# Performance work log

Hardware: AMD Instinct MI355X
Metric: run time of the kernel (lower is better)

Reference implementation:

```python
import jax, jax.numpy as jnp
import numpy as np


def setup_inputs() -> dict:
    key = jax.random.key(0)
    k1, k2 = jax.random.split(key)
    z = jax.random.normal(k1, (16, 128, 32, 32), dtype=jnp.float32)
    e = jax.random.normal(k2, (8192, 128), dtype=jnp.float32)
    log_sigma = jnp.zeros((1,), dtype=jnp.float32)  # init_log_sigma = 0.0
    return {"z": z, "e": e, "log_sigma": log_sigma}


def reference(z, e, log_sigma):
    # z: [B, C, H, W] latents; e: [M, C] codebook; log_sigma: [1]
    B, C, H, W = z.shape
    zf = jnp.transpose(z, (0, 2, 3, 1)).reshape(-1, C)  # [N, C]
    N = zf.shape[0]
    M = e.shape[0]
    T = 1.0  # latent_temp default

    # squared L2 distance via expanded dot products: ||z||^2 + ||e||^2 - 2 z.e
    z_sq = jnp.sum(zf * zf, axis=1, keepdims=True)          # [N, 1]
    e_sq = jnp.sum(e * e, axis=1)[None, :]                  # [1, M]
    dist = jnp.maximum(z_sq + e_sq - 2.0 * (zf @ e.T), 0.0)  # [N, M]

    alpha = -1.0 / (2.0 * jnp.exp(log_sigma[0]) ** 2)
    A = alpha * dist / T                                     # [N, M]

    # np.log(np.e) == 1.0 in the original
    const = 0.5 * C * (2.0 * log_sigma - 1.0)                # [1]
    lse1_loss = -jnp.mean(T * jax.nn.logsumexp(A, axis=1)) + const + jnp.log(float(M))
    lse2_loss = -jnp.mean(T * jax.nn.logsumexp(A, axis=0)) + const + jnp.log(float(N))
    return lse1_loss, lse2_loss
```

## Files before the change

kernel.cpp:

```cpp
#include <hip/hip_runtime.h>
#include <hip/hip_bf16.h>

typedef unsigned short u16;
typedef __attribute__((ext_vector_type(8))) short short8;
typedef __attribute__((ext_vector_type(4))) float float4v;
typedef __attribute__((ext_vector_type(2))) float float2v;

#define N_ROWS 16384
#define M_COLS 8192
#define KDIM   128
#define SHIFT  64.0f
#define STRIPES 64
#define SPLITS  64
#define CHUNKS  4

__device__ inline u16 f2bf(float f) {
  unsigned u = __builtin_bit_cast(unsigned, f);
  unsigned r = (u + 0x7fffu + ((u >> 16) & 1u)) >> 16;
  return (u16)r;
}

__global__ void prep(const float* __restrict__ z, const float* __restrict__ e,
                     u16* __restrict__ zf, u16* __restrict__ ef,
                     float* __restrict__ zsq, float* __restrict__ esq,
                     double* __restrict__ dacc, unsigned* __restrict__ dcnt) {
  if (blockIdx.x < 512) {
    const int b = blockIdx.x >> 5, h = blockIdx.x & 31;
    __shared__ float tile[128 * 33];
    __shared__ float psum[8][32];
    const float* src = z + ((size_t)b * 128 * 32 + h) * 32;
    for (int idx = threadIdx.x; idx < 4096; idx += 256) {
      int c = idx >> 5, w = idx & 31;
      tile[c * 33 + w] = src[c * 1024 + w];
    }
    __syncthreads();
    {
      int w = threadIdx.x & 31, cg = threadIdx.x >> 5;
      float s = 0.f;
#pragma unroll
      for (int cc = 0; cc < 16; ++cc) {
        float v = tile[(cg * 16 + cc) * 33 + w];
        s = fmaf(v, v, s);
      }
      psum[cg][w] = s;
    }
    for (int idx = threadIdx.x; idx < 512; idx += 256) {
      int w = idx >> 4, g = idx & 15;
      short8 v;
#pragma unroll
      for (int cc = 0; cc < 8; ++cc) v[cc] = (short)f2bf(tile[(g * 8 + cc) * 33 + w]);
      *(short8*)&zf[((size_t)b * 1024 + h * 32 + w) * 128 + g * 8] = v;
    }
    __syncthreads();
    if (threadIdx.x < 32) {
      int w = threadIdx.x;
      float s = 0.f;
#pragma unroll
      for (int cg = 0; cg < 8; ++cg) s += psum[cg][w];
      zsq[b * 1024 + h * 32 + w] = s;
    }
  } else {
    if (blockIdx.x == 512 && threadIdx.x == 0) {
      __hip_atomic_store(&dacc[0], 0.0, __ATOMIC_RELAXED, __HIP_MEMORY_SCOPE_AGENT);
      __hip_atomic_store(&dacc[1], 0.0, __ATOMIC_RELAXED, __HIP_MEMORY_SCOPE_AGENT);
      __hip_atomic_store(dcnt, 0u, __ATOMIC_RELAXED, __HIP_MEMORY_SCOPE_AGENT);
    }
    const int gw = ((blockIdx.x - 512) * 256 + threadIdx.x) >> 6;
    const int ln = threadIdx.x & 63;
    for (int r = gw; r < M_COLS; r += 512) {
      float2 v = *(const float2*)&e[r * 128 + ln * 2];
      unsigned pk = (unsigned)f2bf(v.x) | ((unsigned)f2bf(v.y) << 16);
      *(unsigned*)&ef[r * 128 + ln * 2] = pk;
      float s = fmaf(v.x, v.x, v.y * v.y);
#pragma unroll
      for (int sh = 1; sh < 64; sh <<= 1) s += __shfl_xor(s, sh);
      if (ln == 0) esq[r] = s;
    }
  }
}

__global__ __launch_bounds__(256, 3) void gemm_lse(
    const u16* __restrict__ zf, const u16* __restrict__ ef,
    const float* __restrict__ zsq, const float* __restrict__ esq,
    const float* __restrict__ log_sigma,
    float* __restrict__ rpart, float* __restrict__ cpart) {
  __shared__ __align__(16) u16 et[128 * 128];
  __shared__ float colacc[4][128];
  const int tid = threadIdx.x;
  const int ln = tid & 63, wv = tid >> 6;
  const int l15 = ln & 15, q = ln >> 4;
  const int stripe = blockIdx.x, split = blockIdx.y;
  const int colbase = split * 128;

  {
    const u16* efb = ef + (size_t)colbase * 128;
#pragma unroll
    for (int it = 0; it < 8; ++it) {
      int u = it * 256 + tid;
      int r = u >> 4, p_ = u & 15;
      int g = p_ ^ (r & 15);
      __builtin_amdgcn_global_load_lds(
          (const __attribute__((address_space(1))) unsigned int*)(efb + r * 128 + g * 8),
          (__attribute__((address_space(3))) unsigned int*)(et + (it * 256 + wv * 64) * 8),
          16, 0, 0);
    }
  }

  short8 af[4][4];
#pragma unroll
  for (int i = 0; i < 4; ++i)
#pragma unroll
    for (int kk = 0; kk < 4; ++kk)
      af[i][kk] = *(const short8*)(zf +
          (size_t)(stripe * 256 + wv * 64 + i * 16 + l15) * 128 + kk * 32 + q * 8);

  const float lsv = log_sigma[0];
  const float sg = __expf(lsv);
  const float alpha = -0.5f / (sg * sg);
  const float L2E = 1.44269504088896f;
  const float ca = alpha * L2E, cb = SHIFT * L2E, m2ca = -2.0f * ca;
  const float2v m2ca2 = {m2ca, m2ca};

  float2v zb2[4][2];
#pragma unroll
  for (int i = 0; i < 4; ++i) {
    float4v zs = *(const float4v*)(zsq + stripe * 256 + wv * 64 + i * 16 + q * 4);
    zb2[i][0] = (float2v){fmaf(ca, zs[0], cb), fmaf(ca, zs[1], cb)};
    zb2[i][1] = (float2v){fmaf(ca, zs[2], cb), fmaf(ca, zs[3], cb)};
  }

  float2v rs01[4], rs23[4];
#pragma unroll
  for (int i = 0; i < 4; ++i) {
    rs01[i] = (float2v){0.f, 0.f};
    rs23[i] = (float2v){0.f, 0.f};
  }

  __syncthreads();

#pragma unroll 1
  for (int t = 0; t < CHUNKS; ++t) {
    float ebv[2];
#pragma unroll
    for (int j = 0; j < 2; ++j) ebv[j] = ca * esq[colbase + t * 32 + j * 16 + l15];

    const u16* bb = et + t * 32 * 128;

    float4v acc[4][2];
#pragma unroll
    for (int kk = 0; kk < 4; ++kk) {
      short8 bfr[2];
      const int poff = ((kk * 4 + q) ^ l15) * 8;
#pragma unroll
      for (int j = 0; j < 2; ++j)
        bfr[j] = *(const short8*)(bb + (j * 16 + l15) * 128 + poff);
      if (kk == 0) {
#pragma unroll
        for (int i = 0; i < 4; ++i)
#pragma unroll
          for (int j = 0; j < 2; ++j)
            acc[i][j] = __builtin_amdgcn_mfma_f32_16x16x32_bf16(
                af[i][0], bfr[j], (float4v){0.f, 0.f, 0.f, 0.f}, 0, 0, 0);
      } else {
#pragma unroll
        for (int i = 0; i < 4; ++i)
#pragma unroll
          for (int j = 0; j < 2; ++j)
            acc[i][j] = __builtin_amdgcn_mfma_f32_16x16x32_bf16(
                af[i][kk], bfr[j], acc[i][j], 0, 0, 0);
      }
    }

    float2v csv[2];
    csv[0] = (float2v){0.f, 0.f};
    csv[1] = (float2v){0.f, 0.f};

#pragma unroll
    for (int i = 0; i < 4; ++i) {
#pragma unroll
      for (int j = 0; j < 2; ++j) {
        float2v eb2 = {ebv[j], ebv[j]};
        float2v a01 = {acc[i][j][0], acc[i][j][1]};
        float2v a23 = {acc[i][j][2], acc[i][j][3]};
        float2v g01 = a01 * m2ca2 + (zb2[i][0] + eb2);
        float2v g23 = a23 * m2ca2 + (zb2[i][1] + eb2);
        float2v e01 = {__builtin_amdgcn_exp2f(g01.x), __builtin_amdgcn_exp2f(g01.y)};
        float2v e23 = {__builtin_amdgcn_exp2f(g23.x), __builtin_amdgcn_exp2f(g23.y)};
        rs01[i] += e01;
        rs23[i] += e23;
        csv[j] += e01 + e23;
      }
    }
#pragma unroll
    for (int j = 0; j < 2; ++j) {
      float c = csv[j].x + csv[j].y;
      c += __shfl_xor(c, 16);
      c += __shfl_xor(c, 32);
      if (q == 0) colacc[wv][t * 32 + j * 16 + l15] = c;
    }
  }

  __syncthreads();
  if (tid < 128) {
    float s = 0.f;
#pragma unroll
    for (int w = 0; w < 4; ++w) s += colacc[w][tid];
    cpart[(size_t)stripe * M_COLS + colbase + tid] = s;
  }

#pragma unroll
  for (int i = 0; i < 4; ++i)
    for (int s = 1; s < 16; s <<= 1) {
      rs01[i].x += __shfl_xor(rs01[i].x, s);
      rs01[i].y += __shfl_xor(rs01[i].y, s);
      rs23[i].x += __shfl_xor(rs23[i].x, s);
      rs23[i].y += __shfl_xor(rs23[i].y, s);
    }
  if (l15 == 0) {
#pragma unroll
    for (int i = 0; i < 4; ++i) {
      int rbase = stripe * 256 + wv * 64 + i * 16 + q * 4;
      rpart[(size_t)split * N_ROWS + rbase + 0] = rs01[i].x;
      rpart[(size_t)split * N_ROWS + rbase + 1] = rs01[i].y;
      rpart[(size_t)split * N_ROWS + rbase + 2] = rs23[i].x;
      rpart[(size_t)split * N_ROWS + rbase + 3] = rs23[i].y;
    }
  }
}

__global__ void fin(const float* __restrict__ rpart, const float* __restrict__ cpart,
                    const float* __restrict__ log_sigma,
                    double* __restrict__ dacc, unsigned* __restrict__ dcnt,
                    float* __restrict__ out) {
  const int tid = threadIdx.x, b = blockIdx.x;
  double v;
  if (b < 64) {
    int row = b * 256 + tid;
    float s = 0.f;
#pragma unroll
    for (int p = 0; p < SPLITS; ++p) s += rpart[(size_t)p * N_ROWS + row];
    v = (double)logf(s);
  } else {
    int col = (b - 64) * 256 + tid;
    float s = 0.f;
#pragma unroll
    for (int p = 0; p < STRIPES; ++p) s += cpart[(size_t)p * M_COLS + col];
    v = (double)logf(s);
  }
  __shared__ double red[256];
  red[tid] = v;
  __syncthreads();
  for (int s = 128; s > 0; s >>= 1) {
    if (tid < s) red[tid] += red[tid + s];
    __syncthreads();
  }
  if (tid == 0) {
    atomicAdd(&dacc[b < 64 ? 0 : 1], red[0]);
    __threadfence();
    unsigned ticket = atomicAdd(dcnt, 1u);
    if (ticket == 95u) {
      double s1 = atomicAdd(&dacc[0], 0.0);
      double s2 = atomicAdd(&dacc[1], 0.0);
      float lsv = log_sigma[0];
      float cst = 0.5f * 128.0f * (2.0f * lsv - 1.0f);
      out[0] = (float)(-(s1 / N_ROWS - (double)SHIFT)) + cst + logf((float)M_COLS);
      out[1] = (float)(-(s2 / M_COLS - (double)SHIFT)) + cst + logf((float)N_ROWS);
    }
  }
}

extern "C" void kernel_launch(void* const* d_in, const int* in_sizes, int n_in,
                              void* d_out, int out_size, void* d_ws, size_t ws_size,
                              hipStream_t stream) {
  const float* z  = (const float*)d_in[0];
  const float* e  = (const float*)d_in[1];
  const float* ls = (const float*)d_in[2];
  float* out = (float*)d_out;
  char* ws = (char*)d_ws;
  u16*   zf    = (u16*)ws;
  u16*   ef    = (u16*)(ws + (4u << 20));
  float* zsq   = (float*)(ws + (6u << 20));
  float* esq   = (float*)(ws + (6u << 20) + (64u << 10));
  float* rpart = (float*)(ws + (6u << 20) + (96u << 10));
  float* cpart = (float*)(ws + (10u << 20) + (96u << 10));
  double* dacc = (double*)(ws + (12u << 20) + (96u << 10));
  unsigned* dcnt = (unsigned*)(ws + (12u << 20) + (96u << 10) + 16);

  prep<<<dim3(640), dim3(256), 0, stream>>>(z, e, zf, ef, zsq, esq, dacc, dcnt);
  gemm_lse<<<dim3(STRIPES, SPLITS), dim3(256), 0, stream>>>(zf, ef, zsq, esq, ls, rpart, cpart);
  fin<<<dim3(96), dim3(256), 0, stream>>>(rpart, cpart, ls, dacc, dcnt, out);
}
```

Baseline: 153.9 us.

## Halve GEMM-LSE tile to 128x64, raise occupancy, store partial sums as bf16

Each gemm_lse block now covers 128 rows by 64 codebook columns instead of 256x128, giving a 128x128 grid. The smaller LDS tile and register footprint allow launch bounds of 5 blocks per CU. Row and column partial exp-sums are stored as bf16 to offset the doubled count of partials the finalize kernel must read. Risks: more blocks redo the codebook staging and A-fragment loads, and bf16 rounding of the partials reduces accuracy of the final logsumexp.

```diff
diff --git a/kernel.cpp b/kernel.cpp
--- a/kernel.cpp
+++ b/kernel.cpp
@@ -10,14 +10,18 @@
 #define M_COLS 8192
 #define KDIM   128
 #define SHIFT  64.0f
-#define STRIPES 64
-#define SPLITS  64
-#define CHUNKS  4
+#define STRIPES 128
+#define SPLITS  128
+#define CHUNKS  2
 
 __device__ inline u16 f2bf(float f) {
   unsigned u = __builtin_bit_cast(unsigned, f);
   unsigned r = (u + 0x7fffu + ((u >> 16) & 1u)) >> 16;
   return (u16)r;
+}
+__device__ inline float bf2f(u16 h) {
+  unsigned u = ((unsigned)h) << 16;
+  return __builtin_bit_cast(float, u);
 }
 
 __global__ void prep(const float* __restrict__ z, const float* __restrict__ e,
@@ -79,23 +83,23 @@
   }
 }
 
-__global__ __launch_bounds__(256, 3) void gemm_lse(
+__global__ __launch_bounds__(256, 5) void gemm_lse(
     const u16* __restrict__ zf, const u16* __restrict__ ef,
     const float* __restrict__ zsq, const float* __restrict__ esq,
     const float* __restrict__ log_sigma,
-    float* __restrict__ rpart, float* __restrict__ cpart) {
-  __shared__ __align__(16) u16 et[128 * 128];
-  __shared__ float colacc[4][128];
+    u16* __restrict__ rpart, u16* __restrict__ cpart) {
+  __shared__ __align__(16) u16 et[64 * 128];
+  __shared__ float colacc[4][64];
   const int tid = threadIdx.x;
   const int ln = tid & 63, wv = tid >> 6;
   const int l15 = ln & 15, q = ln >> 4;
   const int stripe = blockIdx.x, split = blockIdx.y;
-  const int colbase = split * 128;
+  const int colbase = split * 64;
 
   {
     const u16* efb = ef + (size_t)colbase * 128;
 #pragma unroll
-    for (int it = 0; it < 8; ++it) {
+    for (int it = 0; it < 4; ++it) {
       int u = it * 256 + tid;
       int r = u >> 4, p_ = u & 15;
       int g = p_ ^ (r & 15);
@@ -106,13 +110,13 @@
     }
   }
 
-  short8 af[4][4];
-#pragma unroll
-  for (int i = 0; i < 4; ++i)
+  short8 af[2][4];
+#pragma unroll
+  for (int i = 0; i < 2; ++i)
 #pragma unroll
     for (int kk = 0; kk < 4; ++kk)
       af[i][kk] = *(const short8*)(zf +
-          (size_t)(stripe * 256 + wv * 64 + i * 16 + l15) * 128 + kk * 32 + q * 8);
+          (size_t)(stripe * 128 + wv * 32 + i * 16 + l15) * 128 + kk * 32 + q * 8);
 
   const float lsv = log_sigma[0];
   const float sg = __expf(lsv);
@@ -121,17 +125,17 @@
   const float ca = alpha * L2E, cb = SHIFT * L2E, m2ca = -2.0f * ca;
   const float2v m2ca2 = {m2ca, m2ca};
 
-  float2v zb2[4][2];
-#pragma unroll
-  for (int i = 0; i < 4; ++i) {
-    float4v zs = *(const float4v*)(zsq + stripe * 256 + wv * 64 + i * 16 + q * 4);
+  float2v zb2[2][2];
+#pragma unroll
+  for (int i = 0; i < 2; ++i) {
+    float4v zs = *(const float4v*)(zsq + stripe * 128 + wv * 32 + i * 16 + q * 4);
     zb2[i][0] = (float2v){fmaf(ca, zs[0], cb), fmaf(ca, zs[1], cb)};
     zb2[i][1] = (float2v){fmaf(ca, zs[2], cb), fmaf(ca, zs[3], cb)};
   }
 
-  float2v rs01[4], rs23[4];
-#pragma unroll
-  for (int i = 0; i < 4; ++i) {
+  float2v rs01[2], rs23[2];
+#pragma unroll
+  for (int i = 0; i < 2; ++i) {
     rs01[i] = (float2v){0.f, 0.f};
     rs23[i] = (float2v){0.f, 0.f};
   }
@@ -146,7 +150,7 @@
 
     const u16* bb = et + t * 32 * 128;
 
-    float4v acc[4][2];
+    float4v acc[2][2];
 #pragma unroll
     for (int kk = 0; kk < 4; ++kk) {
       short8 bfr[2];
@@ -156,14 +160,14 @@
         bfr[j] = *(const short8*)(bb + (j * 16 + l15) * 128 + poff);
       if (kk == 0) {
 #pragma unroll
-        for (int i = 0; i < 4; ++i)
+        for (int i = 0; i < 2; ++i)
 #pragma unroll
           for (int j = 0; j < 2; ++j)
             acc[i][j] = __builtin_amdgcn_mfma_f32_16x16x32_bf16(
                 af[i][0], bfr[j], (float4v){0.f, 0.f, 0.f, 0.f}, 0, 0, 0);
       } else {
 #pragma unroll
-        for (int i = 0; i < 4; ++i)
+        for (int i = 0; i < 2; ++i)
 #pragma unroll
           for (int j = 0; j < 2; ++j)
             acc[i][j] = __builtin_amdgcn_mfma_f32_16x16x32_bf16(
@@ -176,14 +180,16 @@
     csv[1] = (float2v){0.f, 0.f};
 
 #pragma unroll
-    for (int i = 0; i < 4; ++i) {
+    for (int i = 0; i < 2; ++i) {
 #pragma unroll
       for (int j = 0; j < 2; ++j) {
         float2v eb2 = {ebv[j], ebv[j]};
+        float2v zbeb01 = zb2[i][0] + eb2;
+        float2v zbeb23 = zb2[i][1] + eb2;
         float2v a01 = {acc[i][j][0], acc[i][j][1]};
         float2v a23 = {acc[i][j][2], acc[i][j][3]};
-        float2v g01 = a01 * m2ca2 + (zb2[i][0] + eb2);
-        float2v g23 = a23 * m2ca2 + (zb2[i][1] + eb2);
+        float2v g01 = a01 * m2ca2 + zbeb01;
+        float2v g23 = a23 * m2ca2 + zbeb23;
         float2v e01 = {__builtin_amdgcn_exp2f(g01.x), __builtin_amdgcn_exp2f(g01.y)};
         float2v e23 = {__builtin_amdgcn_exp2f(g23.x), __builtin_amdgcn_exp2f(g23.y)};
         rs01[i] += e01;
@@ -201,15 +207,15 @@
   }
 
   __syncthreads();
-  if (tid < 128) {
+  if (tid < 64) {
     float s = 0.f;
 #pragma unroll
     for (int w = 0; w < 4; ++w) s += colacc[w][tid];
-    cpart[(size_t)stripe * M_COLS + colbase + tid] = s;
-  }
-
-#pragma unroll
-  for (int i = 0; i < 4; ++i)
+    cpart[(size_t)stripe * M_COLS + colbase + tid] = f2bf(s);
+  }
+
+#pragma unroll
+  for (int i = 0; i < 2; ++i)
     for (int s = 1; s < 16; s <<= 1) {
       rs01[i].x += __shfl_xor(rs01[i].x, s);
       rs01[i].y += __shfl_xor(rs01[i].y, s);
@@ -218,17 +224,17 @@
     }
   if (l15 == 0) {
 #pragma unroll
-    for (int i = 0; i < 4; ++i) {
-      int rbase = stripe * 256 + wv * 64 + i * 16 + q * 4;
-      rpart[(size_t)split * N_ROWS + rbase + 0] = rs01[i].x;
-      rpart[(size_t)split * N_ROWS + rbase + 1] = rs01[i].y;
-      rpart[(size_t)split * N_ROWS + rbase + 2] = rs23[i].x;
-      rpart[(size_t)split * N_ROWS + rbase + 3] = rs23[i].y;
-    }
-  }
-}
-
-__global__ void fin(const float* __restrict__ rpart, const float* __restrict__ cpart,
+    for (int i = 0; i < 2; ++i) {
+      int rbase = stripe * 128 + wv * 32 + i * 16 + q * 4;
+      rpart[(size_t)split * N_ROWS + rbase + 0] = f2bf(rs01[i].x);
+      rpart[(size_t)split * N_ROWS + rbase + 1] = f2bf(rs01[i].y);
+      rpart[(size_t)split * N_ROWS + rbase + 2] = f2bf(rs23[i].x);
+      rpart[(size_t)split * N_ROWS + rbase + 3] = f2bf(rs23[i].y);
+    }
+  }
+}
+
+__global__ void fin(const u16* __restrict__ rpart, const u16* __restrict__ cpart,
                     const float* __restrict__ log_sigma,
                     double* __restrict__ dacc, unsigned* __restrict__ dcnt,
                     float* __restrict__ out) {
@@ -238,13 +244,13 @@
     int row = b * 256 + tid;
     float s = 0.f;
 #pragma unroll
-    for (int p = 0; p < SPLITS; ++p) s += rpart[(size_t)p * N_ROWS + row];
+    for (int p = 0; p < SPLITS; ++p) s += bf2f(rpart[(size_t)p * N_ROWS + row]);
     v = (double)logf(s);
   } else {
     int col = (b - 64) * 256 + tid;
     float s = 0.f;
 #pragma unroll
-    for (int p = 0; p < STRIPES; ++p) s += cpart[(size_t)p * M_COLS + col];
+    for (int p = 0; p < STRIPES; ++p) s += bf2f(cpart[(size_t)p * M_COLS + col]);
     v = (double)logf(s);
   }
   __shared__ double red[256];
@@ -281,8 +287,8 @@
   u16*   ef    = (u16*)(ws + (4u << 20));
   float* zsq   = (float*)(ws + (6u << 20));
   float* esq   = (float*)(ws + (6u << 20) + (64u << 10));
-  float* rpart = (float*)(ws + (6u << 20) + (96u << 10));
-  float* cpart = (float*)(ws + (10u << 20) + (96u << 10));
+  u16*   rpart = (u16*)(ws + (6u << 20) + (96u << 10));
+  u16*   cpart = (u16*)(ws + (10u << 20) + (96u << 10));
   double* dacc = (double*)(ws + (12u << 20) + (96u << 10));
   unsigned* dcnt = (unsigned*)(ws + (12u << 20) + (96u << 10) + 16);
 
```

Result: slower. 170.7 us (+10.9%).
